# Kernel tuning notes

Hardware: AMD Instinct MI355X
Metric: run time of the kernel (lower is better)

## Reference

```python
import jax, jax.numpy as jnp
import numpy as np


def _rotate_nearest(img, theta):
    """Rotate a batch of images (B, C, H, W) counterclockwise by theta radians
    about the image center, nearest-neighbor sampling, zero fill outside
    (matches torchvision rotate defaults: InterpolationMode.NEAREST, expand=False)."""
    B, C, H, W = img.shape
    cy = (H - 1) / 2.0
    cx = (W - 1) / 2.0
    ys = jnp.arange(H, dtype=jnp.float32) - cy
    xs = jnp.arange(W, dtype=jnp.float32) - cx
    yg, xg = jnp.meshgrid(ys, xs, indexing="ij")  # (H, W)
    c = jnp.cos(theta)
    s = jnp.sin(theta)
    # inverse affine map: output pixel -> source pixel
    x_src = c * xg + s * yg + cx
    y_src = -s * xg + c * yg + cy
    xi = jnp.round(x_src).astype(jnp.int32)
    yi = jnp.round(y_src).astype(jnp.int32)
    valid = (xi >= 0) & (xi < W) & (yi >= 0) & (yi < H)
    xi = jnp.clip(xi, 0, W - 1)
    yi = jnp.clip(yi, 0, H - 1)
    out = img[:, :, yi, xi]  # gather -> (B, C, H, W)
    return jnp.where(valid, out, jnp.zeros((), img.dtype))


def reference(image, kernel_size):
    # image: (B, C, H, W, A); A = num_angles
    B, C, H, W, A = image.shape
    angle_increment = 360.0 / A
    offsets = (jnp.arange(A) % kernel_size).astype(jnp.float32)
    # torch code calls rotate(slice, -angle_increment * relative_offset) in degrees
    thetas = jnp.deg2rad(-angle_increment * offsets)  # (A,)
    img_a = jnp.moveaxis(image, -1, 0)  # (A, B, C, H, W)
    rot = jax.vmap(_rotate_nearest, in_axes=(0, 0))(img_a, thetas)  # (A, B, C, H, W)
    rot = jnp.moveaxis(rot, 0, -1)  # (B, C, H, W, A)
    # MaxPool3d(kernel=(1,1,k)) == non-overlapping max over windows of k along angle dim
    pooled = rot.reshape(B, C, H, W, A // kernel_size, kernel_size).max(axis=-1)
    return pooled  # (B, C, H, W, A // kernel_size)


def setup_inputs() -> dict:
    key = jax.random.key(0)
    image = jax.random.normal(key, (8, 16, 128, 128, 24), dtype=jnp.float32)
    return {"image": image, "kernel_size": 4}
```

## Files before the change

kernel.cpp:

```cpp
#include <hip/hip_runtime.h>
#include <math.h>


#pragma clang fp contract(off)

#define HH 128
#define WW 128
#define AA 24
#define GG 6
#define TS 16
#define NWAVE 4

#define GLDS(gp, lp)                                       \
  __builtin_amdgcn_global_load_lds(                        \
      (const __attribute__((address_space(1))) void*)(gp), \
      (__attribute__((address_space(3))) void*)(lp), 4, 0, 0)

template <int K>
__device__ __forceinline__ void ktrig(float& cth, float& sth) {
  float tdeg = -15.0f * (float)K;
  float theta = tdeg * 0.017453292519943295f;
  cth = (float)cos((double)theta);
  sth = (float)sin((double)theta);
}

template <int K, int WK, int HK>
__device__ __forceinline__ void window_k(float xga, float xgb, float yga,
                                         float ygb, int& bx0, int& by0) {
  float cth, sth;
  ktrig<K>(cth, sth);
  float xs00 = cth * xga + sth * yga + 63.5f;
  float xs01 = cth * xga + sth * ygb + 63.5f;
  float xs10 = cth * xgb + sth * yga + 63.5f;
  float xs11 = cth * xgb + sth * ygb + 63.5f;
  float ys00 = (-sth) * xga + cth * yga + 63.5f;
  float ys01 = (-sth) * xga + cth * ygb + 63.5f;
  float ys10 = (-sth) * xgb + cth * yga + 63.5f;
  float ys11 = (-sth) * xgb + cth * ygb + 63.5f;
  float minxs = fminf(fminf(xs00, xs01), fminf(xs10, xs11));
  float minys = fminf(fminf(ys00, ys01), fminf(ys10, ys11));
  bx0 = min(max((int)rintf(minxs), 0), WW - WK);
  by0 = min(max((int)rintf(minys), 0), HH - HK);
}

template <int K, int WK, int HK>
__device__ __forceinline__ void stage_k(const float* sbase, float* lplane,
                                        int bx0, int by0, int wave, int lane) {
  constexpr int LR = WK * GG;
  constexpr int NFULL = LR >> 6;
  constexpr int REM = LR & 63;
  constexpr int NJ = (HK + NWAVE - 1) / NWAVE;
#pragma unroll
  for (int j = 0; j < NJ; ++j) {
    int dy = wave + NWAVE * j;
    dy = dy < HK ? dy : HK - 1;
    const float* row = sbase + ((by0 + dy) * WW + bx0) * AA + K;
    float* lrow = lplane + dy * LR;
#pragma unroll
    for (int c = 0; c < NFULL; ++c) {
      GLDS(row + 4 * (64 * c + lane), lrow + 64 * c);
    }
    if (REM && lane < REM) {
      GLDS(row + 4 * (64 * NFULL + lane), lrow + 64 * NFULL);
    }
  }
}

template <int K, int WK, int HK>
__device__ __forceinline__ void gather_k(const float* lplane, int bx0, int by0,
                                         float xg, float yg, float* r) {
  float cth, sth;
  ktrig<K>(cth, sth);
  float xs = cth * xg + sth * yg + 63.5f;
  float ys = (-sth) * xg + cth * yg + 63.5f;
  int xi = (int)rintf(xs);
  int yi = (int)rintf(ys);
  bool valid = ((unsigned)xi < (unsigned)WW) & ((unsigned)yi < (unsigned)HH);
  int dxr = min(max(xi - bx0, 0), WK - 1);
  int dyr = min(max(yi - by0, 0), HK - 1);
  const float2* lp = (const float2*)(lplane + dyr * (WK * GG) + dxr * GG);
  float2 v01 = lp[0];
  float2 v23 = lp[1];
  float2 v45 = lp[2];
  r[0] = fmaxf(r[0], valid ? v01.x : 0.0f);
  r[1] = fmaxf(r[1], valid ? v01.y : 0.0f);
  r[2] = fmaxf(r[2], valid ? v23.x : 0.0f);
  r[3] = fmaxf(r[3], valid ? v23.y : 0.0f);
  r[4] = fmaxf(r[4], valid ? v45.x : 0.0f);
  r[5] = fmaxf(r[5], valid ? v45.y : 0.0f);
}

__global__ __launch_bounds__(256, 6) void glp_rotation_pool_kernel(
    const float* __restrict__ img, float* __restrict__ out) {
  __shared__ __align__(16) float buf0[2904];
  __shared__ __align__(16) float buf1[3174];

  int blk = blockIdx.x;
  int xcd = blk & 7;
  int i = blk >> 3;
  int bc = (xcd << 4) | (i >> 6);
  int tile = i & 63;
  int ty = (tile >> 3) << 4;
  int tx = (tile & 7) << 4;

  int tid = threadIdx.x;
  int px = tid & 15;
  int py = tid >> 4;
  int wave = tid >> 6;
  int lane = tid & 63;

  const float* sbase = img + (size_t)bc * (HH * WW * AA);

  float xg = (float)(tx + px) - 63.5f;
  float yg = (float)(ty + py) - 63.5f;
  float xga = (float)tx - 63.5f, xgb = (float)(tx + TS - 1) - 63.5f;
  float yga = (float)ty - 63.5f, ygb = (float)(ty + TS - 1) - 63.5f;

  int bx0_0, by0_0, bx0_1, by0_1, bx0_2, by0_2, bx0_3, by0_3;
  window_k<0, 16, 16>(xga, xgb, yga, ygb, bx0_0, by0_0);
  window_k<1, 20, 20>(xga, xgb, yga, ygb, bx0_1, by0_1);
  window_k<2, 22, 22>(xga, xgb, yga, ygb, bx0_2, by0_2);
  window_k<3, 23, 23>(xga, xgb, yga, ygb, bx0_3, by0_3);

  float r[6] = {-INFINITY, -INFINITY, -INFINITY,
                -INFINITY, -INFINITY, -INFINITY};

  stage_k<0, 16, 16>(sbase, buf0, bx0_0, by0_0, wave, lane);
  stage_k<1, 20, 20>(sbase, buf1, bx0_1, by0_1, wave, lane);
  asm volatile("s_waitcnt vmcnt(10)" ::: "memory");
  __builtin_amdgcn_sched_barrier(0);
  __builtin_amdgcn_s_barrier();
  __builtin_amdgcn_sched_barrier(0);
  gather_k<0, 16, 16>(buf0, bx0_0, by0_0, xg, yg, r);
  asm volatile("s_waitcnt lgkmcnt(0)" ::: "memory");
  __builtin_amdgcn_sched_barrier(0);
  __builtin_amdgcn_s_barrier();
  __builtin_amdgcn_sched_barrier(0);
  stage_k<2, 22, 22>(sbase, buf0, bx0_2, by0_2, wave, lane);
  asm volatile("s_waitcnt vmcnt(18)" ::: "memory");
  __builtin_amdgcn_sched_barrier(0);
  __builtin_amdgcn_s_barrier();
  __builtin_amdgcn_sched_barrier(0);
  gather_k<1, 20, 20>(buf1, bx0_1, by0_1, xg, yg, r);
  asm volatile("s_waitcnt lgkmcnt(0)" ::: "memory");
  __builtin_amdgcn_sched_barrier(0);
  __builtin_amdgcn_s_barrier();
  __builtin_amdgcn_sched_barrier(0);
  stage_k<3, 23, 23>(sbase, buf1, bx0_3, by0_3, wave, lane);
  asm volatile("s_waitcnt vmcnt(18)" ::: "memory");
  __builtin_amdgcn_sched_barrier(0);
  __builtin_amdgcn_s_barrier();
  __builtin_amdgcn_sched_barrier(0);
  gather_k<2, 22, 22>(buf0, bx0_2, by0_2, xg, yg, r);
  asm volatile("s_waitcnt vmcnt(0) lgkmcnt(0)" ::: "memory");
  __builtin_amdgcn_sched_barrier(0);
  __builtin_amdgcn_s_barrier();
  __builtin_amdgcn_sched_barrier(0);
  gather_k<3, 23, 23>(buf1, bx0_3, by0_3, xg, yg, r);

  size_t opix =
      ((size_t)bc * (HH * WW) + (size_t)(ty + py) * WW + (tx + px)) * GG;
  float2* op = (float2*)&out[opix];
  op[0] = make_float2(r[0], r[1]);
  op[1] = make_float2(r[2], r[3]);
  op[2] = make_float2(r[4], r[5]);
}

extern "C" void kernel_launch(void* const* d_in, const int* in_sizes, int n_in,
                              void* d_out, int out_size, void* d_ws,
                              size_t ws_size, hipStream_t stream) {
  const float* img = (const float*)d_in[0];
  float* out = (float*)d_out;
  dim3 grid(128 * 64);
  dim3 block(256);
  glp_rotation_pool_kernel<<<grid, block, 0, stream>>>(img, out);
}
```

Baseline: 333.8 us.

## Issue all four angle stagings up front into separate LDS buffers

```diff
diff --git a/kernel.cpp b/kernel.cpp
--- a/kernel.cpp
+++ b/kernel.cpp
@@ -50,18 +50,20 @@
   constexpr int NFULL = LR >> 6;
   constexpr int REM = LR & 63;
   constexpr int NJ = (HK + NWAVE - 1) / NWAVE;
+  static_assert(NFULL <= 2, "extend the ladder");
 #pragma unroll
   for (int j = 0; j < NJ; ++j) {
     int dy = wave + NWAVE * j;
     dy = dy < HK ? dy : HK - 1;
     const float* row = sbase + ((by0 + dy) * WW + bx0) * AA + K;
+    const float* g0 = row + 4 * lane;
     float* lrow = lplane + dy * LR;
-#pragma unroll
-    for (int c = 0; c < NFULL; ++c) {
-      GLDS(row + 4 * (64 * c + lane), lrow + 64 * c);
-    }
-    if (REM && lane < REM) {
-      GLDS(row + 4 * (64 * NFULL + lane), lrow + 64 * NFULL);
+    if constexpr (NFULL >= 1) GLDS(g0, lrow);
+    if constexpr (NFULL >= 2) GLDS(g0 + 256, lrow + 64);
+    if constexpr (REM != 0) {
+      if (lane < REM) {
+        GLDS(g0 + 256 * NFULL, lrow + 64 * NFULL);
+      }
     }
   }
 }
@@ -90,10 +92,12 @@
   r[5] = fmaxf(r[5], valid ? v45.y : 0.0f);
 }
 
-__global__ __launch_bounds__(256, 6) void glp_rotation_pool_kernel(
+__global__ __launch_bounds__(256, 4) void glp_rotation_pool_kernel(
     const float* __restrict__ img, float* __restrict__ out) {
-  __shared__ __align__(16) float buf0[2904];
-  __shared__ __align__(16) float buf1[3174];
+  __shared__ __align__(16) float bufA[1536];
+  __shared__ __align__(16) float bufB[2400];
+  __shared__ __align__(16) float bufC[2904];
+  __shared__ __align__(16) float bufD[3174];
 
   int blk = blockIdx.x;
   int xcd = blk & 7;
@@ -125,38 +129,34 @@
   float r[6] = {-INFINITY, -INFINITY, -INFINITY,
                 -INFINITY, -INFINITY, -INFINITY};
 
-  stage_k<0, 16, 16>(sbase, buf0, bx0_0, by0_0, wave, lane);
-  stage_k<1, 20, 20>(sbase, buf1, bx0_1, by0_1, wave, lane);
-  asm volatile("s_waitcnt vmcnt(10)" ::: "memory");
+  stage_k<0, 16, 16>(sbase, bufA, bx0_0, by0_0, wave, lane);
+  stage_k<1, 20, 20>(sbase, bufB, bx0_1, by0_1, wave, lane);
+  stage_k<2, 22, 22>(sbase, bufC, bx0_2, by0_2, wave, lane);
+  stage_k<3, 23, 23>(sbase, bufD, bx0_3, by0_3, wave, lane);
+
+  asm volatile("s_waitcnt vmcnt(46)" ::: "memory");
   __builtin_amdgcn_sched_barrier(0);
   __builtin_amdgcn_s_barrier();
   __builtin_amdgcn_sched_barrier(0);
-  gather_k<0, 16, 16>(buf0, bx0_0, by0_0, xg, yg, r);
-  asm volatile("s_waitcnt lgkmcnt(0)" ::: "memory");
+  gather_k<0, 16, 16>(bufA, bx0_0, by0_0, xg, yg, r);
+
+  asm volatile("s_waitcnt vmcnt(36)" ::: "memory");
   __builtin_amdgcn_sched_barrier(0);
   __builtin_amdgcn_s_barrier();
   __builtin_amdgcn_sched_barrier(0);
-  stage_k<2, 22, 22>(sbase, buf0, bx0_2, by0_2, wave, lane);
+  gather_k<1, 20, 20>(bufB, bx0_1, by0_1, xg, yg, r);
+
   asm volatile("s_waitcnt vmcnt(18)" ::: "memory");
   __builtin_amdgcn_sched_barrier(0);
   __builtin_amdgcn_s_barrier();
   __builtin_amdgcn_sched_barrier(0);
-  gather_k<1, 20, 20>(buf1, bx0_1, by0_1, xg, yg, r);
-  asm volatile("s_waitcnt lgkmcnt(0)" ::: "memory");
+  gather_k<2, 22, 22>(bufC, bx0_2, by0_2, xg, yg, r);
+
+  asm volatile("s_waitcnt vmcnt(0)" ::: "memory");
   __builtin_amdgcn_sched_barrier(0);
   __builtin_amdgcn_s_barrier();
   __builtin_amdgcn_sched_barrier(0);
-  stage_k<3, 23, 23>(sbase, buf1, bx0_3, by0_3, wave, lane);
-  asm volatile("s_waitcnt vmcnt(18)" ::: "memory");
-  __builtin_amdgcn_sched_barrier(0);
-  __builtin_amdgcn_s_barrier();
-  __builtin_amdgcn_sched_barrier(0);
-  gather_k<2, 22, 22>(buf0, bx0_2, by0_2, xg, yg, r);
-  asm volatile("s_waitcnt vmcnt(0) lgkmcnt(0)" ::: "memory");
-  __builtin_amdgcn_sched_barrier(0);
-  __builtin_amdgcn_s_barrier();
-  __builtin_amdgcn_sched_barrier(0);
-  gather_k<3, 23, 23>(buf1, bx0_3, by0_3, xg, yg, r);
+  gather_k<3, 23, 23>(bufD, bx0_3, by0_3, xg, yg, r);
 
   size_t opix =
       ((size_t)bc * (HH * WW) + (size_t)(ty + py) * WW + (tx + px)) * GG;
```

Measured after the change: 337.8 us. About the same (+1.2%).
